# Kernel optimization log

Hardware: AMD Instinct MI355X
Metric: run time of the kernel (lower is better)

The kernel has to match this reference:

```python
import jax, jax.numpy as jnp
import numpy as np

NUM_LABELS = 17
MARGIN = 1.0
IGNORE = -100


def setup_inputs() -> dict:
    key = jax.random.key(0)
    k1, k2, k3 = jax.random.split(key, 3)
    B, S, H = 64, 1024, 384
    embeddings = jax.random.normal(k1, (B, S, H), dtype=jnp.float32)
    classifier_w = jax.random.normal(k2, (NUM_LABELS, H), dtype=jnp.float32) * 0.02
    classifier_b = jnp.zeros((NUM_LABELS,), dtype=jnp.float32)
    labels = jax.random.randint(k3, (B, S), 0, NUM_LABELS, dtype=jnp.int64 if jax.config.jax_enable_x64 else jnp.int32)
    attention_mask = jnp.ones((B, S), dtype=jnp.int32)
    return {"embeddings": embeddings, "classifier_w": classifier_w,
            "classifier_b": classifier_b, "labels": labels,
            "attention_mask": attention_mask}


def _total_loss(embeddings, W, b, labels, mask):
    B, S, H = embeddings.shape
    N = B * S
    fe = embeddings.reshape(N, H)          # [N,H] flattened tokens
    fl = labels.reshape(N)
    fm = mask.reshape(N) > 0

    # ----- cross entropy (ignore_index=-100), matches F.cross_entropy mean -----
    logits = fe @ W.T + b                  # [N, L]
    logp = jax.nn.log_softmax(logits, axis=-1)
    safe = jnp.where(fl == IGNORE, 0, fl)
    nll = -jnp.take_along_axis(logp, safe[:, None], axis=1)[:, 0]
    ce_valid = fl != IGNORE
    ce = jnp.sum(jnp.where(ce_valid, nll, 0.0)) / jnp.maximum(jnp.sum(ce_valid), 1)

    # ----- quadruplet loss (deterministic sampling: earliest occurrences) -----
    idx = jnp.arange(N)
    BIG = N  # sentinel index > any real index
    is_ent = fm & (fl > 0)
    non_ent = fm & (fl == 0)
    d_i = jnp.min(jnp.where(non_ent, idx, BIG))   # first non-entity token
    has_non = jnp.any(non_ent)

    def per_type(t):
        m = is_ent & (fl == t)
        order = jnp.sort(jnp.where(m, idx, BIG))
        a_i, p_i = order[0], order[1]             # anchor / positive = first two occurrences
        cnt = jnp.sum(m)
        other = is_ent & (fl != t)
        n_i = jnp.min(jnp.where(other, idx, BIG))  # negative = first other-type entity
        ok = (cnt >= 2) & jnp.any(other) & has_non
        return a_i, p_i, n_i, ok

    types = jnp.arange(1, NUM_LABELS)
    a_i, p_i, n_i, ok = jax.vmap(per_type)(types)  # each [L-1]
    clip = lambda i: jnp.clip(i, 0, N - 1)
    A = fe[clip(a_i)]
    P = fe[clip(p_i)]
    Ng = fe[clip(n_i)]
    D = fe[clip(d_i)][None, :]
    eps = 1e-6  # torch F.pairwise_distance eps added to the difference
    dist = lambda x, y: jnp.sqrt(jnp.sum((x - y + eps) ** 2, axis=-1))
    pd, nd, dd = dist(A, P), dist(A, Ng), dist(A, D)
    ql = jax.nn.relu(pd - nd + MARGIN) + jax.nn.relu(pd - dd + 2.0 * MARGIN)
    qcnt = jnp.sum(ok)
    quad = jnp.sum(jnp.where(ok, ql, 0.0)) / jnp.maximum(qcnt, 1)
    quad = jnp.where(qcnt > 0, quad, 0.0)

    # ----- context loss: adjacent same-entity tokens, mean-per-pair MSE -----
    l0, l1 = labels[:, :-1], labels[:, 1:]
    pair = (l0 != IGNORE) & (l0 == l1) & (l0 > 0)
    mse = jnp.mean((embeddings[:, :-1] - embeddings[:, 1:]) ** 2, axis=-1)  # [B,S-1]
    pc = jnp.sum(pair)
    ctx = jnp.sum(jnp.where(pair, mse, 0.0)) / jnp.maximum(pc, 1)
    ctx = jnp.where(pc > 0, ctx, 0.0)

    return ce + 0.5 * quad + 0.1 * ctx


def reference(embeddings, classifier_w, classifier_b, labels, attention_mask):
    return _total_loss(embeddings, classifier_w, classifier_b, labels, attention_mask)
```

## Files before the change

kernel.cpp:

```cpp
#include <hip/hip_runtime.h>

#define NL 17
#define IGN (-100)
#define HD 384
#define NSEQ 1024
#define NT 65536
#define BIGI NT
#define TPB 256
#define NBLK (NT / TPB)
#define NCHUNK 12
#define CF4 8

typedef unsigned int u32;
typedef __attribute__((ext_vector_type(8))) short bf16x8;
typedef __attribute__((ext_vector_type(16))) float f32x16;

#define GLOAD_LDS16(g, l) __builtin_amdgcn_global_load_lds(                    \
    (const __attribute__((address_space(1))) u32*)(g),                         \
    (__attribute__((address_space(3))) u32*)(l), 16, 0, 0)

__device__ __forceinline__ u32 cvtpk(float lo, float hi) {
  u32 u;
  asm("v_cvt_pk_bf16_f32 %0, %1, %2" : "=v"(u) : "v"(lo), "v"(hi));
  return u;
}

struct WS {
  float ce_part[NBLK];
  float ctx_part[NBLK];
  int   ce_cnt[NBLK];
  int   ctx_cnt[NBLK];
  int   blk_a[NBLK][16];
  int   blk_p[NBLK][16];
  int   blk_c[NBLK][16];
  int   blk_d[NBLK];
};

__global__ __launch_bounds__(256, 1) void k_main(const float* __restrict__ emb,
                                                 const float* __restrict__ cw,
                                                 const float* __restrict__ cb,
                                                 const int* __restrict__ labels,
                                                 const int* __restrict__ mask,
                                                 WS* __restrict__ ws) {
  __shared__ float4 tile[4][TPB * CF4];
  __shared__ float4 sW4[NL * (HD / 4)];
  __shared__ float sce[4], sctx[4];
  __shared__ int   svc[4], spc[4];
  __shared__ float sbctx;
  __shared__ int   sbcnt;
  __shared__ int   sla[16], slp[16], slc[16], sld;

  const int tid = threadIdx.x, lane = tid & 63, wid = tid >> 6;
  const int b = blockIdx.x;
  const int token = b * TPB + tid;

  const float4* cw4 = (const float4*)cw;
  for (int i = tid; i < NL * (HD / 4); i += TPB) {
    int c = i / (HD / 4), q = i % (HD / 4);
    sW4[c * (HD / 4) + (q ^ (c & 7))] = cw4[i];
  }
  if (tid < 16) { sla[tid] = BIGI; slp[tid] = BIGI; slc[tid] = 0; }
  if (tid == 16) sld = BIGI;
  __syncthreads();

  const int rb  = tid >> 3;
  const int c4  = tid & 7;
  const int gc4 = c4 ^ (rb & 7);
  const float* src0 = emb + (size_t)b * TPB * HD + (size_t)rb * HD + gc4 * 4;
  const int wbase = __builtin_amdgcn_readfirstlane(wid * 64);

#pragma unroll
  for (int k = 0; k < CF4; ++k)
    GLOAD_LDS16(src0 + (size_t)k * 32 * HD, &tile[0][k * 256 + wbase]);
#pragma unroll
  for (int k = 0; k < CF4; ++k)
    GLOAD_LDS16(src0 + 32 + (size_t)k * 32 * HD, &tile[1][k * 256 + wbase]);

  const int cls = lane & 31;
  const int kh  = lane >> 5;
  const int clsS = (cls < NL) ? cls : 0;
  const int row0 = wid * 64 + (lane & 31);
  const int row1 = row0 + 32;
  const int r0 = tid;
  const int r1 = (tid < TPB - 1) ? tid + 1 : tid;
  const int x0 = r0 & 7, x1 = r1 & 7;

  f32x16 d0 = {0.f}, d1 = {0.f};
  float ctxacc = 0.f;

  auto bfrag = [&](const float4* tb, int row, int s) -> bf16x8 {
    int g0 = (s * 4 + kh * 2) ^ (row & 7);
    int g1 = (s * 4 + kh * 2 + 1) ^ (row & 7);
    float4 f0 = tb[(row << 3) | g0];
    float4 f1 = tb[(row << 3) | g1];
    union { u32 u[4]; bf16x8 v; } X;
    X.u[0] = cvtpk(f0.x, f0.y); X.u[1] = cvtpk(f0.z, f0.w);
    X.u[2] = cvtpk(f1.x, f1.y); X.u[3] = cvtpk(f1.z, f1.w);
    return X.v;
  };

  auto afrag = [&](int ch, int s) -> bf16x8 {
    union { u32 u[4]; bf16x8 v; } X;
    if (cls < NL) {
      int qa = (ch * 2 + s) * 4 + kh * 2;
      float4 f0 = sW4[clsS * (HD / 4) + ((qa) ^ (cls & 7))];
      float4 f1 = sW4[clsS * (HD / 4) + ((qa + 1) ^ (cls & 7))];
      X.u[0] = cvtpk(f0.x, f0.y); X.u[1] = cvtpk(f0.z, f0.w);
      X.u[2] = cvtpk(f1.x, f1.y); X.u[3] = cvtpk(f1.z, f1.w);
    } else {
      X.u[0] = 0; X.u[1] = 0; X.u[2] = 0; X.u[3] = 0;
    }
    return X.v;
  };

  auto compute = [&](int ch, const float4* tb) {
#pragma unroll
    for (int q = 0; q < CF4; ++q) {
      float4 a  = tb[(r0 << 3) | (q ^ x0)];
      float4 nb = tb[(r1 << 3) | (q ^ x1)];
      float e0 = a.x - nb.x, e1 = a.y - nb.y, e2 = a.z - nb.z, e3 = a.w - nb.w;
      ctxacc = fmaf(e0, e0, fmaf(e1, e1, fmaf(e2, e2, fmaf(e3, e3, ctxacc))));
    }
    bf16x8 a0 = afrag(ch, 0), a1 = afrag(ch, 1);
    bf16x8 b00 = bfrag(tb, row0, 0), b01 = bfrag(tb, row0, 1);
    bf16x8 b10 = bfrag(tb, row1, 0), b11 = bfrag(tb, row1, 1);
    d0 = __builtin_amdgcn_mfma_f32_32x32x16_bf16(a0, b00, d0, 0, 0, 0);
    d0 = __builtin_amdgcn_mfma_f32_32x32x16_bf16(a1, b01, d0, 0, 0, 0);
    d1 = __builtin_amdgcn_mfma_f32_32x32x16_bf16(a0, b10, d1, 0, 0, 0);
    d1 = __builtin_amdgcn_mfma_f32_32x32x16_bf16(a1, b11, d1, 0, 0, 0);
  };

#pragma unroll 1
  for (int ch = 0; ch < NCHUNK - 2; ++ch) {
    const float* srcn = src0 + (size_t)(ch + 2) * 32;
    float4* dstb = tile[(ch + 2) & 3];
#pragma unroll
    for (int k = 0; k < CF4; ++k)
      GLOAD_LDS16(srcn + (size_t)k * 32 * HD, &dstb[k * 256 + wbase]);
    asm volatile("s_waitcnt vmcnt(16)" ::: "memory");
    __builtin_amdgcn_sched_barrier(0);
    __builtin_amdgcn_s_barrier();
    __builtin_amdgcn_sched_barrier(0);
    compute(ch, tile[ch & 3]);
  }
  asm volatile("s_waitcnt vmcnt(8)" ::: "memory");
  __builtin_amdgcn_sched_barrier(0);
  __builtin_amdgcn_s_barrier();
  __builtin_amdgcn_sched_barrier(0);
  compute(NCHUNK - 2, tile[(NCHUNK - 2) & 3]);
  asm volatile("s_waitcnt vmcnt(0)" ::: "memory");
  __builtin_amdgcn_sched_barrier(0);
  __builtin_amdgcn_s_barrier();
  __builtin_amdgcn_sched_barrier(0);
  compute(NCHUNK - 1, tile[(NCHUNK - 1) & 3]);
  __syncthreads();

  float* logit = (float*)&tile[0][0];
#pragma unroll
  for (int r = 0; r < 16; ++r) {
    int row = (r & 3) + 8 * (r >> 2) + 4 * kh;
    if (row < NL) {
      logit[(wid * 64 + (lane & 31)) * 21 + row] = d0[r];
      logit[(wid * 64 + 32 + (lane & 31)) * 21 + row] = d1[r];
    }
  }
  __syncthreads();

  int lb = labels[token];
  int mk = mask[token];
  int lbm = (mk > 0) ? lb : IGN;
  if (lbm == 0) atomicMin(&sld, token);
  else if (lbm >= 1 && lbm < NL) { atomicMin(&sla[lbm - 1], token); atomicAdd(&slc[lbm - 1], 1); }
  __syncthreads();
  if (lbm >= 1 && lbm < NL && token > sla[lbm - 1]) atomicMin(&slp[lbm - 1], token);

  float lg[NL];
#pragma unroll
  for (int c = 0; c < NL; ++c) lg[c] = logit[tid * 21 + c] + cb[c];
  float m = lg[0];
#pragma unroll
  for (int c = 1; c < NL; ++c) m = fmaxf(m, lg[c]);
  float s = 0.f;
#pragma unroll
  for (int c = 0; c < NL; ++c) s += __expf(lg[c] - m);
  float lse = m + __logf(s);
  int safe = (lb == IGN) ? 0 : lb;
  float ll = 0.f;
#pragma unroll
  for (int c = 0; c < NL; ++c) ll = (c == safe) ? lg[c] : ll;
  bool valid = (lb != IGN);
  float cev = valid ? (lse - ll) : 0.f;

  int nlb = (tid < TPB - 1) ? labels[token + 1] : IGN;
  bool pair = (tid < TPB - 1) && valid && (lb == nlb) && (lb > 0);
  float ctxv = pair ? ctxacc * (1.0f / HD) : 0.f;

  unsigned long long bv = __ballot(valid);
  unsigned long long bp = __ballot(pair);
#pragma unroll
  for (int off = 32; off; off >>= 1) {
    cev  += __shfl_xor(cev, off, 64);
    ctxv += __shfl_xor(ctxv, off, 64);
  }
  if (lane == 0) { sce[wid] = cev; sctx[wid] = ctxv; svc[wid] = __popcll(bv); spc[wid] = __popcll(bp); }

  if (wid == 3) {
    int t = b * TPB + TPB - 1;
    float bc = 0.f; int bn = 0;
    if (((t + 1) & (NSEQ - 1)) != 0) {
      int l0 = labels[t], l1 = labels[t + 1];
      if (l0 != IGN && l0 == l1 && l0 > 0) {
        const float* ra = emb + (size_t)t * HD;
        const float* rbp = ra + HD;
        float a = 0.f;
#pragma unroll
        for (int j = 0; j < 6; ++j) {
          float dd = ra[lane + 64 * j] - rbp[lane + 64 * j];
          a = fmaf(dd, dd, a);
        }
#pragma unroll
        for (int off = 32; off; off >>= 1) a += __shfl_xor(a, off, 64);
        bc = a * (1.0f / HD); bn = 1;
      }
    }
    if (lane == 0) { sbctx = bc; sbcnt = bn; }
  }
  __syncthreads();
  if (tid < 16) {
    ws->blk_a[b][tid] = sla[tid];
    ws->blk_p[b][tid] = slp[tid];
    ws->blk_c[b][tid] = slc[tid];
  }
  if (tid == 16) ws->blk_d[b] = sld;
  if (tid == 0) {
    ws->ce_part[b]  = sce[0] + sce[1] + sce[2] + sce[3];
    ws->ce_cnt[b]   = svc[0] + svc[1] + svc[2] + svc[3];
    ws->ctx_part[b] = sctx[0] + sctx[1] + sctx[2] + sctx[3] + sbctx;
    ws->ctx_cnt[b]  = spc[0] + spc[1] + spc[2] + spc[3] + sbcnt;
  }
}

__global__ __launch_bounds__(256) void k_final(const float* __restrict__ emb,
                                               WS* __restrict__ ws,
                                               float* __restrict__ out) {
  __shared__ double rce[256], rctx[256];
  __shared__ int rvc[256], rpc[256], rd[256];
  __shared__ int M1[256], M2[256], CN[256];
  __shared__ int ga[16], gp[16], gc[16];
  __shared__ float qs[4]; __shared__ int qc[4];
  const int tid = threadIdx.x, lane = tid & 63, wid = tid >> 6;

  rce[tid]  = ws->ce_part[tid];
  rctx[tid] = ws->ctx_part[tid];
  rvc[tid]  = ws->ce_cnt[tid];
  rpc[tid]  = ws->ctx_cnt[tid];
  rd[tid]   = ws->blk_d[tid];

  {
    const int type = tid & 15, seg = tid >> 4;
    int m1 = BIGI, m2 = BIGI, cnt = 0;
#pragma unroll 4
    for (int k = 0; k < 16; ++k) {
      int bb = seg * 16 + k;
      int x = ws->blk_a[bb][type];
      if (x < m1) { m2 = m1; m1 = x; } else if (x < m2) { m2 = x; }
      int y = ws->blk_p[bb][type];
      if (y < m1) { m2 = m1; m1 = y; } else if (y < m2) { m2 = y; }
      cnt += ws->blk_c[bb][type];
    }
    M1[tid] = m1; M2[tid] = m2; CN[tid] = cnt;
  }
  __syncthreads();
  for (int s = 128; s > 0; s >>= 1) {
    if (tid < s) {
      rce[tid] += rce[tid + s]; rctx[tid] += rctx[tid + s];
      rvc[tid] += rvc[tid + s]; rpc[tid] += rpc[tid + s];
      rd[tid] = min(rd[tid], rd[tid + s]);
    }
    __syncthreads();
  }
  if (tid < 16) {
    int m1 = BIGI, m2 = BIGI, cnt = 0;
    for (int seg = 0; seg < 16; ++seg) {
      int a1 = M1[seg * 16 + tid], a2 = M2[seg * 16 + tid];
      int n1 = min(m1, a1);
      int n2 = min(max(m1, a1), min(m2, a2));
      m1 = n1; m2 = n2;
      cnt += CN[seg * 16 + tid];
    }
    ga[tid] = m1; gp[tid] = m2; gc[tid] = cnt;
  }
  __syncthreads();

  const int gd = rd[0];
  float qsum = 0.f; int qcnt = 0;
  for (int tt = 0; tt < 4; ++tt) {
    int t = wid * 4 + tt;
    int a = ga[t], p = gp[t], c = gc[t];
    int nmin = BIGI;
#pragma unroll
    for (int u = 0; u < 16; ++u) if (u != t) nmin = min(nmin, ga[u]);
    bool ok = (c >= 2) && (nmin < BIGI) && (gd < BIGI);
    if (ok) {
      const float* A  = emb + (size_t)min(a, NT - 1) * HD;
      const float* P  = emb + (size_t)min(p, NT - 1) * HD;
      const float* Ng = emb + (size_t)min(nmin, NT - 1) * HD;
      const float* D  = emb + (size_t)min(gd, NT - 1) * HD;
      float sap = 0.f, san = 0.f, sad = 0.f;
#pragma unroll
      for (int j = 0; j < 6; ++j) {
        int idx = lane + 64 * j;
        float av = A[idx];
        float d1 = av - P[idx] + 1e-6f;  sap = fmaf(d1, d1, sap);
        float d2 = av - Ng[idx] + 1e-6f; san = fmaf(d2, d2, san);
        float d3 = av - D[idx] + 1e-6f;  sad = fmaf(d3, d3, sad);
      }
#pragma unroll
      for (int off = 32; off; off >>= 1) {
        sap += __shfl_xor(sap, off, 64);
        san += __shfl_xor(san, off, 64);
        sad += __shfl_xor(sad, off, 64);
      }
      float pd = sqrtf(sap), nd = sqrtf(san), dd = sqrtf(sad);
      qsum += fmaxf(pd - nd + 1.0f, 0.f) + fmaxf(pd - dd + 2.0f, 0.f);
      qcnt += 1;
    }
  }
  if (lane == 0) { qs[wid] = qsum; qc[wid] = qcnt; }
  __syncthreads();
  if (tid == 0) {
    double tq = (double)qs[0] + qs[1] + qs[2] + qs[3];
    int tqc = qc[0] + qc[1] + qc[2] + qc[3];
    double ce   = rce[0] / (double)max(rvc[0], 1);
    double ctx  = (rpc[0] > 0) ? rctx[0] / (double)rpc[0] : 0.0;
    double quad = (tqc > 0) ? tq / (double)tqc : 0.0;
    out[0] = (float)(ce + 0.5 * quad + 0.1 * ctx);
  }
}

extern "C" void kernel_launch(void* const* d_in, const int* in_sizes, int n_in,
                              void* d_out, int out_size, void* d_ws, size_t ws_size,
                              hipStream_t stream) {
  const float* emb    = (const float*)d_in[0];
  const float* cw     = (const float*)d_in[1];
  const float* cb     = (const float*)d_in[2];
  const int*   labels = (const int*)d_in[3];
  const int*   mask   = (const int*)d_in[4];
  WS* ws = (WS*)d_ws;
  float* out = (float*)d_out;

  k_main <<<NBLK, 256, 0, stream>>>(emb, cw, cb, labels, mask, ws);
  k_final<<<1, 256, 0, stream>>>(emb, ws, out);
}
```

Measured before the change: 36.37 us.

## Fuse final reduction into main kernel via last-block atomic and prepack W to bf16

The separate single-block finalize kernel is removed. Each block now increments an atomic counter, and the last block to finish performs the global reduction and the quadruplet loss in scratch LDS reused from the tile buffer. A memset of the counter is added before the launch. Separately, the classifier weights are converted once to bf16 into a padded LDS array, so the MFMA A-fragments become a single 16-byte load instead of per-chunk fp32 loads plus conversions. This trades a kernel launch gap for an extra memset node and a tail of serial work in one block.

```diff
diff --git a/kernel.cpp b/kernel.cpp
--- a/kernel.cpp
+++ b/kernel.cpp
@@ -10,8 +10,10 @@
 #define NBLK (NT / TPB)
 #define NCHUNK 12
 #define CF4 8
+#define WPAD 392
 
 typedef unsigned int u32;
+typedef unsigned short u16;
 typedef __attribute__((ext_vector_type(8))) short bf16x8;
 typedef __attribute__((ext_vector_type(16))) float f32x16;
 
@@ -26,6 +28,8 @@
 }
 
 struct WS {
+  u32   cnt;
+  u32   pad0[15];
   float ce_part[NBLK];
   float ctx_part[NBLK];
   int   ce_cnt[NBLK];
@@ -41,23 +45,24 @@
                                                  const float* __restrict__ cb,
                                                  const int* __restrict__ labels,
                                                  const int* __restrict__ mask,
-                                                 WS* __restrict__ ws) {
+                                                 WS* __restrict__ ws,
+                                                 float* __restrict__ out) {
   __shared__ float4 tile[4][TPB * CF4];
-  __shared__ float4 sW4[NL * (HD / 4)];
-  __shared__ float sce[4], sctx[4];
-  __shared__ int   svc[4], spc[4];
-  __shared__ float sbctx;
-  __shared__ int   sbcnt;
-  __shared__ int   sla[16], slp[16], slc[16], sld;
+  __shared__ u16    sWh[NL * WPAD];
+  __shared__ float  sce[4], sctx[4];
+  __shared__ int    svc[4], spc[4];
+  __shared__ float  sbctx;
+  __shared__ int    sbcnt;
+  __shared__ int    sla[16], slp[16], slc[16], sld, slast;
 
   const int tid = threadIdx.x, lane = tid & 63, wid = tid >> 6;
   const int b = blockIdx.x;
   const int token = b * TPB + tid;
 
-  const float4* cw4 = (const float4*)cw;
-  for (int i = tid; i < NL * (HD / 4); i += TPB) {
-    int c = i / (HD / 4), q = i % (HD / 4);
-    sW4[c * (HD / 4) + (q ^ (c & 7))] = cw4[i];
+  for (int i = tid; i < NL * (HD / 2); i += TPB) {
+    int c = i / (HD / 2), p = i % (HD / 2);
+    u32 pk = cvtpk(cw[c * HD + 2 * p], cw[c * HD + 2 * p + 1]);
+    *(u32*)&sWh[c * WPAD + 2 * p] = pk;
   }
   if (tid < 16) { sla[tid] = BIGI; slp[tid] = BIGI; slc[tid] = 0; }
   if (tid == 16) sld = BIGI;
@@ -69,12 +74,15 @@
   const float* src0 = emb + (size_t)b * TPB * HD + (size_t)rb * HD + gc4 * 4;
   const int wbase = __builtin_amdgcn_readfirstlane(wid * 64);
 
-#pragma unroll
-  for (int k = 0; k < CF4; ++k)
-    GLOAD_LDS16(src0 + (size_t)k * 32 * HD, &tile[0][k * 256 + wbase]);
-#pragma unroll
-  for (int k = 0; k < CF4; ++k)
-    GLOAD_LDS16(src0 + 32 + (size_t)k * 32 * HD, &tile[1][k * 256 + wbase]);
+  auto issue = [&](int c) {
+    const float* s = src0 + (size_t)c * 32;
+    float4* d = tile[c & 3];
+#pragma unroll
+    for (int k = 0; k < CF4; ++k)
+      GLOAD_LDS16(s + (size_t)k * 32 * HD, &d[k * 256 + wbase]);
+  };
+
+  issue(0); issue(1);
 
   const int cls = lane & 31;
   const int kh  = lane >> 5;
@@ -88,6 +96,13 @@
   f32x16 d0 = {0.f}, d1 = {0.f};
   float ctxacc = 0.f;
 
+  auto afrag = [&](int ch, int s) -> bf16x8 {
+    if (cls < NL)
+      return *(const bf16x8*)&sWh[clsS * WPAD + ch * 32 + s * 16 + kh * 8];
+    union { u32 u[4]; bf16x8 v; } Z;
+    Z.u[0] = 0; Z.u[1] = 0; Z.u[2] = 0; Z.u[3] = 0;
+    return Z.v;
+  };
   auto bfrag = [&](const float4* tb, int row, int s) -> bf16x8 {
     int g0 = (s * 4 + kh * 2) ^ (row & 7);
     int g1 = (s * 4 + kh * 2 + 1) ^ (row & 7);
@@ -99,20 +114,6 @@
     return X.v;
   };
 
-  auto afrag = [&](int ch, int s) -> bf16x8 {
-    union { u32 u[4]; bf16x8 v; } X;
-    if (cls < NL) {
-      int qa = (ch * 2 + s) * 4 + kh * 2;
-      float4 f0 = sW4[clsS * (HD / 4) + ((qa) ^ (cls & 7))];
-      float4 f1 = sW4[clsS * (HD / 4) + ((qa + 1) ^ (cls & 7))];
-      X.u[0] = cvtpk(f0.x, f0.y); X.u[1] = cvtpk(f0.z, f0.w);
-      X.u[2] = cvtpk(f1.x, f1.y); X.u[3] = cvtpk(f1.z, f1.w);
-    } else {
-      X.u[0] = 0; X.u[1] = 0; X.u[2] = 0; X.u[3] = 0;
-    }
-    return X.v;
-  };
-
   auto compute = [&](int ch, const float4* tb) {
 #pragma unroll
     for (int q = 0; q < CF4; ++q) {
@@ -132,11 +133,7 @@
 
 #pragma unroll 1
   for (int ch = 0; ch < NCHUNK - 2; ++ch) {
-    const float* srcn = src0 + (size_t)(ch + 2) * 32;
-    float4* dstb = tile[(ch + 2) & 3];
-#pragma unroll
-    for (int k = 0; k < CF4; ++k)
-      GLOAD_LDS16(srcn + (size_t)k * 32 * HD, &dstb[k * 256 + wbase]);
+    issue(ch + 2);
     asm volatile("s_waitcnt vmcnt(16)" ::: "memory");
     __builtin_amdgcn_sched_barrier(0);
     __builtin_amdgcn_s_barrier();
@@ -238,24 +235,37 @@
     ws->ctx_part[b] = sctx[0] + sctx[1] + sctx[2] + sctx[3] + sbctx;
     ws->ctx_cnt[b]  = spc[0] + spc[1] + spc[2] + spc[3] + sbcnt;
   }
-}
-
-__global__ __launch_bounds__(256) void k_final(const float* __restrict__ emb,
-                                               WS* __restrict__ ws,
-                                               float* __restrict__ out) {
-  __shared__ double rce[256], rctx[256];
-  __shared__ int rvc[256], rpc[256], rd[256];
-  __shared__ int M1[256], M2[256], CN[256];
-  __shared__ int ga[16], gp[16], gc[16];
-  __shared__ float qs[4]; __shared__ int qc[4];
-  const int tid = threadIdx.x, lane = tid & 63, wid = tid >> 6;
-
-  rce[tid]  = ws->ce_part[tid];
-  rctx[tid] = ws->ctx_part[tid];
-  rvc[tid]  = ws->ce_cnt[tid];
-  rpc[tid]  = ws->ctx_cnt[tid];
-  rd[tid]   = ws->blk_d[tid];
-
+
+  __threadfence();
+  __syncthreads();
+  if (tid == 0) {
+    u32 v = atomicAdd(&ws->cnt, 1u);
+    slast = (v == (u32)(NBLK - 1));
+  }
+  __syncthreads();
+  if (!slast) return;
+  __threadfence();
+
+  char* scr = (char*)&tile[0][0];
+  double* Rce  = (double*)scr;
+  double* Rctx = (double*)(scr + 2048);
+  int* Rvc = (int*)(scr + 4096);
+  int* Rpc = (int*)(scr + 5120);
+  int* Rd  = (int*)(scr + 6144);
+  int* M1  = (int*)(scr + 7168);
+  int* M2  = (int*)(scr + 8192);
+  int* CN  = (int*)(scr + 9216);
+  int* Ga  = (int*)(scr + 10240);
+  int* Gp  = (int*)(scr + 10304);
+  int* Gc  = (int*)(scr + 10368);
+  float* Qs = (float*)(scr + 10432);
+  int* Qc  = (int*)(scr + 10448);
+
+  Rce[tid] = ws->ce_part[tid];
+  Rctx[tid] = ws->ctx_part[tid];
+  Rvc[tid] = ws->ce_cnt[tid];
+  Rpc[tid] = ws->ctx_cnt[tid];
+  Rd[tid]  = ws->blk_d[tid];
   {
     const int type = tid & 15, seg = tid >> 4;
     int m1 = BIGI, m2 = BIGI, cnt = 0;
@@ -271,11 +281,11 @@
     M1[tid] = m1; M2[tid] = m2; CN[tid] = cnt;
   }
   __syncthreads();
-  for (int s = 128; s > 0; s >>= 1) {
-    if (tid < s) {
-      rce[tid] += rce[tid + s]; rctx[tid] += rctx[tid + s];
-      rvc[tid] += rvc[tid + s]; rpc[tid] += rpc[tid + s];
-      rd[tid] = min(rd[tid], rd[tid + s]);
+  for (int st = 128; st > 0; st >>= 1) {
+    if (tid < st) {
+      Rce[tid] += Rce[tid + st]; Rctx[tid] += Rctx[tid + st];
+      Rvc[tid] += Rvc[tid + st]; Rpc[tid] += Rpc[tid + st];
+      Rd[tid] = min(Rd[tid], Rd[tid + st]);
     }
     __syncthreads();
   }
@@ -288,18 +298,18 @@
       m1 = n1; m2 = n2;
       cnt += CN[seg * 16 + tid];
     }
-    ga[tid] = m1; gp[tid] = m2; gc[tid] = cnt;
-  }
-  __syncthreads();
-
-  const int gd = rd[0];
+    Ga[tid] = m1; Gp[tid] = m2; Gc[tid] = cnt;
+  }
+  __syncthreads();
+
+  const int gd = Rd[0];
   float qsum = 0.f; int qcnt = 0;
   for (int tt = 0; tt < 4; ++tt) {
     int t = wid * 4 + tt;
-    int a = ga[t], p = gp[t], c = gc[t];
+    int a = Ga[t], p = Gp[t], c = Gc[t];
     int nmin = BIGI;
 #pragma unroll
-    for (int u = 0; u < 16; ++u) if (u != t) nmin = min(nmin, ga[u]);
+    for (int u = 0; u < 16; ++u) if (u != t) nmin = min(nmin, Ga[u]);
     bool ok = (c >= 2) && (nmin < BIGI) && (gd < BIGI);
     if (ok) {
       const float* A  = emb + (size_t)min(a, NT - 1) * HD;
@@ -326,13 +336,13 @@
       qcnt += 1;
     }
   }
-  if (lane == 0) { qs[wid] = qsum; qc[wid] = qcnt; }
+  if (lane == 0) { Qs[wid] = qsum; Qc[wid] = qcnt; }
   __syncthreads();
   if (tid == 0) {
-    double tq = (double)qs[0] + qs[1] + qs[2] + qs[3];
-    int tqc = qc[0] + qc[1] + qc[2] + qc[3];
-    double ce   = rce[0] / (double)max(rvc[0], 1);
-    double ctx  = (rpc[0] > 0) ? rctx[0] / (double)rpc[0] : 0.0;
+    double tq = (double)Qs[0] + Qs[1] + Qs[2] + Qs[3];
+    int tqc = Qc[0] + Qc[1] + Qc[2] + Qc[3];
+    double ce   = Rce[0] / (double)max(Rvc[0], 1);
+    double ctx  = (Rpc[0] > 0) ? Rctx[0] / (double)Rpc[0] : 0.0;
     double quad = (tqc > 0) ? tq / (double)tqc : 0.0;
     out[0] = (float)(ce + 0.5 * quad + 0.1 * ctx);
   }
@@ -349,6 +359,6 @@
   WS* ws = (WS*)d_ws;
   float* out = (float*)d_out;
 
-  k_main <<<NBLK, 256, 0, stream>>>(emb, cw, cb, labels, mask, ws);
-  k_final<<<1, 256, 0, stream>>>(emb, ws, out);
+  hipMemsetAsync(d_ws, 0, 4, stream);
+  k_main<<<NBLK, TPB, 0, stream>>>(emb, cw, cb, labels, mask, ws, out);
 }
```

New measurement: 57.28 us. 57.5% more time.
